# Optimization experiments

Measured on AMD Instinct MI355X. Metric: run time of the kernel, lower is better.

The kernel has to match this reference:

```python
import jax, jax.numpy as jnp
import numpy as np

B, T, E, H = 4, 1024, 1024, 16
D = E // H  # head_dim = 64


def setup_inputs() -> dict:
    key = jax.random.key(0)
    ks = jax.random.split(key, 6)
    s = 0.02  # realistic init scale for stable softmax
    return {
        "hidden_states": jax.random.normal(ks[0], (B, T, E), jnp.float32),
        "attention_mask": jnp.zeros((B, 1, T, T), jnp.float32),
        "Wq": jax.random.normal(ks[1], (E, E), jnp.float32) * s,
        "bq": jnp.zeros((E,), jnp.float32),
        "Wk": jax.random.normal(ks[2], (E, E), jnp.float32) * s,
        "bk": jnp.zeros((E,), jnp.float32),
        "Wv": jax.random.normal(ks[3], (E, E), jnp.float32) * s,
        "bv": jnp.zeros((E,), jnp.float32),
        "Wo": jax.random.normal(ks[4], (E, E), jnp.float32) * s,
        "bo": jnp.zeros((E,), jnp.float32),
    }


def reference(hidden_states, attention_mask, Wq, bq, Wk, bk, Wv, bv, Wo, bo):
    b, t, e = hidden_states.shape
    scaling = jnp.asarray(D, hidden_states.dtype) ** -0.5
    # q_proj weights/bias are pre-scaled in the module; equivalent to scaling q output
    q = (hidden_states @ Wq.T + bq) * scaling      # [B,T,E]
    k = hidden_states @ Wk.T + bk                   # self-attention path (no cache)
    v = hidden_states @ Wv.T + bv
    q = q.reshape(b, t, H, D)
    k = k.reshape(b, t, H, D)
    v = v.reshape(b, t, H, D)
    # bmm(q, k^T): [B,H,T,S] score matrix (materialized, as in the original)
    scores = jnp.einsum("bthd,bshd->bhts", q, k) + attention_mask
    probs = jax.nn.softmax(scores, axis=-1)
    ctx = jnp.einsum("bhts,bshd->bthd", probs, v).reshape(b, t, e)
    return ctx @ Wo.T + bo
```

## Files before the change

### kernel.cpp

```cpp
#include <hip/hip_runtime.h>
#include <math.h>

#define BB 4
#define TT 1024
#define EE 1024
#define HH 16
#define DD 64
#define KDIM 1024
#define N_HS (4096 * 1024)
#define N_W  (1024 * 1024)
#define NQKV (BB * HH * TT * DD)
#define LOG2E 1.44269504088896340736f

typedef _Float16 f16x8 __attribute__((ext_vector_type(8)));
typedef _Float16 f16x4 __attribute__((ext_vector_type(4)));
typedef float    f32x4 __attribute__((ext_vector_type(4)));

__device__ __forceinline__ unsigned short f2h(float x) {
    _Float16 h = (_Float16)x;
    return __builtin_bit_cast(unsigned short, h);
}
__device__ __forceinline__ void split_h(float x, unsigned short& hi, unsigned short& lo) {
    _Float16 h = (_Float16)x;
    hi = __builtin_bit_cast(unsigned short, h);
    lo = f2h(x - (float)h);
}

__device__ __forceinline__ void gload16(const void* g, void* l) {
    __builtin_amdgcn_global_load_lds(
        (const __attribute__((address_space(1))) void*)g,
        (__attribute__((address_space(3))) void*)l, 16, 0, 0);
}

__global__ __launch_bounds__(256)
void split_kernel(const float* __restrict__ hs,
                  const float* __restrict__ Wq, const float* __restrict__ Wk,
                  const float* __restrict__ Wv, const float* __restrict__ Wo,
                  unsigned short* __restrict__ ws)
{
    const int u = blockIdx.x * 256 + threadIdx.x;
    const float* src;
    unsigned short* dst;
    if (u < (N_HS / 4)) {
        src = hs + (size_t)u * 4;
        dst = ws + (size_t)u * 4;
    } else {
        int v = u - N_HS / 4;
        int wsel = v >> 18;
        int wo   = v & 0x3FFFF;
        const float* Wsrc = (wsel == 0) ? Wq : (wsel == 1) ? Wk : (wsel == 2) ? Wv : Wo;
        src = Wsrc + (size_t)wo * 4;
        dst = ws + (size_t)N_HS + (size_t)wsel * N_W + (size_t)wo * 4;
    }
    float4 x = *(const float4*)src;
    ushort4 h4;
    h4.x = f2h(x.x); h4.y = f2h(x.y); h4.z = f2h(x.z); h4.w = f2h(x.w);
    *(ushort4*)dst = h4;
}

__global__ __launch_bounds__(256)
void mtrans_kernel(const float* __restrict__ mask, float* __restrict__ mt)
{
    __shared__ float Ts[64][65];
    const int b  = blockIdx.y;
    const int m0 = (blockIdx.x & 15) * 64;
    const int n0 = (blockIdx.x >> 4) * 64;
    const float* src = mask + ((size_t)b * TT + m0) * TT + n0;
    float*       dst = mt   + ((size_t)b * TT + n0) * TT + m0;
    const int tid = threadIdx.x;
#pragma unroll
    for (int i = 0; i < 4; i++) {
        int id = tid + i * 256;
        int r = id >> 4, c = id & 15;
        float4 v = *(const float4*)(src + (size_t)r * TT + c * 4);
        Ts[r][c * 4 + 0] = v.x; Ts[r][c * 4 + 1] = v.y;
        Ts[r][c * 4 + 2] = v.z; Ts[r][c * 4 + 3] = v.w;
    }
    __syncthreads();
#pragma unroll
    for (int i = 0; i < 4; i++) {
        int id = tid + i * 256;
        int d = id >> 4, c = id & 15;
        float4 o;
        o.x = Ts[c * 4 + 0][d] * LOG2E;
        o.y = Ts[c * 4 + 1][d] * LOG2E;
        o.z = Ts[c * 4 + 2][d] * LOG2E;
        o.w = Ts[c * 4 + 3][d] * LOG2E;
        *(float4*)(dst + (size_t)d * TT + c * 4) = o;
    }
}

__global__ __launch_bounds__(256)
void qkv_kernel(const unsigned short* __restrict__ hsp,
                const unsigned short* __restrict__ wqp,
                const float* __restrict__ bq, const float* __restrict__ bk,
                const float* __restrict__ bv,
                unsigned short* __restrict__ qkvb)
{
    __shared__ unsigned short Ah[128 * 32], Bh[128 * 32];

    const int widx  = blockIdx.x >> 3;
    const int nbase = (blockIdx.x & 7) * 128;
    const int mbase = blockIdx.y * 128;
    const unsigned short* Wp = wqp + (size_t)widx * N_W;
    const float* bias = (widx == 0) ? bq : (widx == 1) ? bk : bv;
    unsigned short* dst = qkvb + (size_t)widx * NQKV;
    const float scale = (widx == 0) ? 0.125f * LOG2E : 1.0f;

    const int tid  = threadIdx.x;
    const int w    = tid >> 6;
    const int lane = tid & 63;
    const int quad = lane >> 4;
    const int l16  = lane & 15;
    const int wm   = (w >> 1) * 64;
    const int wn   = (w & 1) * 64;

    f32x4 acc[4][4];
#pragma unroll
    for (int i = 0; i < 4; i++)
#pragma unroll
        for (int j = 0; j < 4; j++) acc[i][j] = (f32x4)0.f;

#pragma unroll 1
    for (int kt = 0; kt < KDIM; kt += 32) {
        __syncthreads();
#pragma unroll
        for (int i = 0; i < 2; i++) {
            int u = tid + i * 256;
            int r = u >> 2, c = u & 3;
            int q = c ^ ((r >> 1) & 3);
            gload16(hsp + (size_t)(mbase + r) * KDIM + kt + q * 8, &Ah[u * 8]);
            gload16(Wp  + (size_t)(nbase + r) * KDIM + kt + q * 8, &Bh[u * 8]);
        }
        __syncthreads();

        f16x8 af[4], bfr[4];
#pragma unroll
        for (int i = 0; i < 4; i++) {
            int r = wm + i * 16 + l16;
            af[i] = *(const f16x8*)&Ah[(r * 4 + (quad ^ ((r >> 1) & 3))) * 8];
        }
#pragma unroll
        for (int j = 0; j < 4; j++) {
            int r = wn + j * 16 + l16;
            bfr[j] = *(const f16x8*)&Bh[(r * 4 + (quad ^ ((r >> 1) & 3))) * 8];
        }
#pragma unroll
        for (int i = 0; i < 4; i++)
#pragma unroll
            for (int j = 0; j < 4; j++)
                acc[i][j] = __builtin_amdgcn_mfma_f32_16x16x32_f16(af[i], bfr[j], acc[i][j], 0, 0, 0);
    }

#pragma unroll
    for (int j = 0; j < 4; j++) {
        int n = nbase + wn + j * 16 + l16;
        int h = n >> 6, d = n & 63;
        float bj = bias[n];
#pragma unroll
        for (int i = 0; i < 4; i++)
#pragma unroll
            for (int rr = 0; rr < 4; rr++) {
                int m = mbase + wm + i * 16 + quad * 4 + rr;
                int b = m >> 10, t = m & 1023;
                dst[(((size_t)(b * HH + h) * TT + t) * DD + d)] =
                    f2h((acc[i][j][rr] + bj) * scale);
            }
    }
}

__global__ __launch_bounds__(256)
void vtrans_kernel(const unsigned short* __restrict__ vp,
                   unsigned short* __restrict__ vtp)
{
    __shared__ unsigned short Ts[64 * 72];
    const int bh = blockIdx.y;
    const int t0 = blockIdx.x * 64;
    const unsigned short* src = vp  + (size_t)bh * TT * DD + (size_t)t0 * DD;
    unsigned short*       dst = vtp + (size_t)bh * DD * TT + t0;
    const int tid = threadIdx.x;

#pragma unroll
    for (int i = 0; i < 2; i++) {
        int id = tid + i * 256;
        int r = id >> 3, c = id & 7;
        *(uint4*)&Ts[r * 72 + c * 8] = *(const uint4*)(src + (size_t)r * DD + c * 8);
    }
    __syncthreads();
#pragma unroll
    for (int i = 0; i < 2; i++) {
        int id = tid + i * 256;
        int d = id >> 3, c = id & 7;
        unsigned short tmp[8];
#pragma unroll
        for (int j = 0; j < 8; j++) tmp[j] = Ts[(c * 8 + j) * 72 + d];
        uint4 o;
        o.x = (unsigned int)tmp[0] | ((unsigned int)tmp[1] << 16);
        o.y = (unsigned int)tmp[2] | ((unsigned int)tmp[3] << 16);
        o.z = (unsigned int)tmp[4] | ((unsigned int)tmp[5] << 16);
        o.w = (unsigned int)tmp[6] | ((unsigned int)tmp[7] << 16);
        *(uint4*)(dst + (size_t)d * TT + c * 8) = o;
    }
}

__global__ __launch_bounds__(256)
void outproj_kernel(const unsigned short* __restrict__ ctxh,
                    const unsigned short* __restrict__ ctxl,
                    const unsigned short* __restrict__ wop,
                    const float* __restrict__ bo, float* __restrict__ out)
{
    __shared__ unsigned short Ach[64 * 32], Acl[64 * 32], Bh[128 * 32];

    const int nbase = blockIdx.x * 128;
    const int mbase = blockIdx.y * 64;

    const int tid  = threadIdx.x;
    const int w    = tid >> 6;
    const int lane = tid & 63;
    const int quad = lane >> 4;
    const int l16  = lane & 15;
    const int wm   = (w >> 1) * 32;
    const int wn   = (w & 1) * 64;

    f32x4 acc[2][4];
#pragma unroll
    for (int i = 0; i < 2; i++)
#pragma unroll
        for (int j = 0; j < 4; j++) acc[i][j] = (f32x4)0.f;

#pragma unroll 1
    for (int kt = 0; kt < KDIM; kt += 32) {
        __syncthreads();
        {
            int r = tid >> 2, c = tid & 3;
            int q = c ^ ((r >> 1) & 3);
            size_t ga = (size_t)(mbase + r) * KDIM + kt + q * 8;
            gload16(ctxh + ga, &Ach[tid * 8]);
            gload16(ctxl + ga, &Acl[tid * 8]);
        }
#pragma unroll
        for (int i = 0; i < 2; i++) {
            int u = tid + i * 256;
            int r = u >> 2, c = u & 3;
            int q = c ^ ((r >> 1) & 3);
            gload16(wop + (size_t)(nbase + r) * KDIM + kt + q * 8, &Bh[u * 8]);
        }
        __syncthreads();

        f16x8 ah[2], al[2], bfr[4];
#pragma unroll
        for (int i = 0; i < 2; i++) {
            int r = wm + i * 16 + l16;
            int slot = (r * 4 + (quad ^ ((r >> 1) & 3))) * 8;
            ah[i] = *(const f16x8*)&Ach[slot];
            al[i] = *(const f16x8*)&Acl[slot];
        }
#pragma unroll
        for (int j = 0; j < 4; j++) {
            int r = wn + j * 16 + l16;
            bfr[j] = *(const f16x8*)&Bh[(r * 4 + (quad ^ ((r >> 1) & 3))) * 8];
        }
#pragma unroll
        for (int i = 0; i < 2; i++)
#pragma unroll
            for (int j = 0; j < 4; j++) {
                acc[i][j] = __builtin_amdgcn_mfma_f32_16x16x32_f16(ah[i], bfr[j], acc[i][j], 0, 0, 0);
                acc[i][j] = __builtin_amdgcn_mfma_f32_16x16x32_f16(al[i], bfr[j], acc[i][j], 0, 0, 0);
            }
    }

#pragma unroll
    for (int j = 0; j < 4; j++) {
        int n = nbase + wn + j * 16 + l16;
        float bj = bo[n];
#pragma unroll
        for (int i = 0; i < 2; i++)
#pragma unroll
            for (int rr = 0; rr < 4; rr++) {
                int m = mbase + wm + i * 16 + quad * 4 + rr;
                out[(size_t)m * EE + n] = acc[i][j][rr] + bj;
            }
    }
}

__global__ __launch_bounds__(256)
void attn_kernel(const unsigned short* __restrict__ qp_, const unsigned short* __restrict__ kp_,
                 const unsigned short* __restrict__ vtp_,
                 const float* __restrict__ mtp,
                 unsigned short* __restrict__ ctxh, unsigned short* __restrict__ ctxl)
{
    __shared__ unsigned short Ks[2][64 * 64];
    __shared__ unsigned short Vt[2][64 * 64];

    const int bh = blockIdx.y;
    const int b  = bh >> 4;
    const int h  = bh & 15;
    const int m0 = blockIdx.x * 64;
    const size_t hoff = (size_t)bh * TT * DD;
    const unsigned short* qhp = qp_ + hoff;
    const unsigned short* khp = kp_ + hoff;
    const unsigned short* vtp = vtp_ + hoff;
    const float* mb = mtp + (size_t)b * TT * TT;

    const int tid  = threadIdx.x;
    const int w    = tid >> 6;
    const int lane = tid & 63;
    const int quad = lane >> 4;
    const int l16  = lane & 15;
    const int m    = m0 + w * 16 + l16;

    f16x8 qf[2];
#pragma unroll
    for (int s = 0; s < 2; s++)
        qf[s] = *(const f16x8*)(qhp + (size_t)m * DD + s * 32 + quad * 8);

    f32x4 o2[4];
#pragma unroll
    for (int u = 0; u < 4; u++) o2[u] = (f32x4)0.f;
    float m_i = -INFINITY, l_i = 0.f;

#pragma unroll
    for (int i = 0; i < 2; i++) {
        int u = tid + i * 256;
        int r = u >> 3, cp = u & 7;
        int c = cp ^ (r & 7);
        gload16(khp + (size_t)r * DD + c * 8, &Ks[0][u * 8]);
        gload16(vtp + (size_t)r * TT + c * 8, &Vt[0][u * 8]);
    }
    __syncthreads();

#pragma unroll 2
    for (int it = 0; it < 16; ++it) {
        const int n0  = it * 64;
        const int cur = it & 1;

        f32x4 st[4];
#pragma unroll
        for (int t = 0; t < 4; t++)
#pragma unroll
            for (int r = 0; r < 4; r++)
                st[t][r] = mb[(size_t)(n0 + 16 * t + quad * 4 + r) * TT + m];

        if (it < 15) {
#pragma unroll
            for (int i = 0; i < 2; i++) {
                int u = tid + i * 256;
                int r = u >> 3, cp = u & 7;
                int c = cp ^ (r & 7);
                gload16(khp + (size_t)(n0 + 64 + r) * DD + c * 8, &Ks[cur ^ 1][u * 8]);
                gload16(vtp + (size_t)r * TT + n0 + 64 + c * 8,   &Vt[cur ^ 1][u * 8]);
            }
        }

        __builtin_amdgcn_s_setprio(1);
#pragma unroll
        for (int s = 0; s < 2; s++)
#pragma unroll
            for (int t = 0; t < 4; t++) {
                int R = 16 * t + l16;
                const f16x8 kf = *(const f16x8*)&Ks[cur][(R * 8 + ((s * 4 + quad) ^ (R & 7))) * 8];
                st[t] = __builtin_amdgcn_mfma_f32_16x16x32_f16(kf, qf[s], st[t], 0, 0, 0);
            }
        __builtin_amdgcn_s_setprio(0);

        float rm0 = fmaxf(fmaxf(st[0][0], st[0][1]), fmaxf(st[0][2], st[0][3]));
        float rm1 = fmaxf(fmaxf(st[1][0], st[1][1]), fmaxf(st[1][2], st[1][3]));
        float rm2 = fmaxf(fmaxf(st[2][0], st[2][1]), fmaxf(st[2][2], st[2][3]));
        float rm3 = fmaxf(fmaxf(st[3][0], st[3][1]), fmaxf(st[3][2], st[3][3]));
        float rm  = fmaxf(fmaxf(rm0, rm1), fmaxf(rm2, rm3));
        rm = fmaxf(rm, __shfl_xor(rm, 16));
        rm = fmaxf(rm, __shfl_xor(rm, 32));
        float mn    = fmaxf(m_i, rm);
        float alpha = exp2f(m_i - mn);
        m_i = mn;
        float rs = 0.f;
#pragma unroll
        for (int t = 0; t < 4; t++)
#pragma unroll
            for (int r = 0; r < 4; r++) {
                float p = exp2f(st[t][r] - mn);
                st[t][r] = p;
                rs += p;
            }
        rs += __shfl_xor(rs, 16);
        rs += __shfl_xor(rs, 32);
        l_i = l_i * alpha + rs;

        f16x4 pb[4];
#pragma unroll
        for (int t = 0; t < 4; t++) {
            f16x4 pv;
            pv[0] = (_Float16)st[t][0]; pv[1] = (_Float16)st[t][1];
            pv[2] = (_Float16)st[t][2]; pv[3] = (_Float16)st[t][3];
            pb[t] = pv;
        }

#pragma unroll
        for (int u = 0; u < 4; u++)
#pragma unroll
            for (int rr = 0; rr < 4; rr++) o2[u][rr] *= alpha;

        __builtin_amdgcn_s_setprio(1);
#pragma unroll
        for (int u = 0; u < 4; u++) {
            int R = 16 * u + l16;
#pragma unroll
            for (int t = 0; t < 4; t++) {
                const f16x4 vv = *(const f16x4*)&Vt[cur][(R * 8 + ((2 * t + (quad >> 1)) ^ (R & 7))) * 8 + (quad & 1) * 4];
                o2[u] = __builtin_amdgcn_mfma_f32_16x16x16f16(vv, pb[t], o2[u], 0, 0, 0);
            }
        }
        __builtin_amdgcn_s_setprio(0);

        __syncthreads();
    }

    float inv = 1.0f / l_i;
#pragma unroll
    for (int u = 0; u < 4; u++)
#pragma unroll
        for (int rr = 0; rr < 4; rr++) {
            float val = o2[u][rr] * inv;
            unsigned short hi, lo;
            split_h(val, hi, lo);
            size_t off = ((size_t)(b * TT + m)) * EE + h * DD + u * 16 + quad * 4 + rr;
            ctxh[off] = hi;
            ctxl[off] = lo;
        }
}

extern "C" void kernel_launch(void* const* d_in, const int* in_sizes, int n_in,
                              void* d_out, int out_size, void* d_ws, size_t ws_size,
                              hipStream_t stream)
{
    const float* hs   = (const float*)d_in[0];
    const float* mask = (const float*)d_in[1];
    const float* Wq   = (const float*)d_in[2];
    const float* bq   = (const float*)d_in[3];
    const float* Wk   = (const float*)d_in[4];
    const float* bk   = (const float*)d_in[5];
    const float* Wv   = (const float*)d_in[6];
    const float* bv   = (const float*)d_in[7];
    const float* Wo   = (const float*)d_in[8];
    const float* bo   = (const float*)d_in[9];
    float* out = (float*)d_out;

    unsigned short* ws   = (unsigned short*)d_ws;
    unsigned short* hsp  = ws;
    unsigned short* wqp  = ws + (size_t)N_HS;
    unsigned short* wop  = wqp + 3 * (size_t)N_W;
    unsigned short* qkvb = wqp + 4 * (size_t)N_W;
    unsigned short* qp   = qkvb;
    unsigned short* kp   = qp + (size_t)NQKV;
    unsigned short* vp   = kp + (size_t)NQKV;
    unsigned short* ctxh = ws;
    unsigned short* ctxl = qkvb + 3 * (size_t)NQKV;
    unsigned short* vtp  = ctxl + (size_t)N_HS;
    float*          mtp  = (float*)(vtp + (size_t)NQKV);

    split_kernel<<<8192, 256, 0, stream>>>(hs, Wq, Wk, Wv, Wo, ws);
    mtrans_kernel<<<dim3(256, BB), 256, 0, stream>>>(mask, mtp);
    qkv_kernel<<<dim3(24, 32), 256, 0, stream>>>(hsp, wqp, bq, bk, bv, qkvb);
    vtrans_kernel<<<dim3(TT / 64, BB * HH), 256, 0, stream>>>(vp, vtp);
    attn_kernel<<<dim3(TT / 64, BB * HH), 256, 0, stream>>>(qp, kp, vtp, mtp, ctxh, ctxl);
    outproj_kernel<<<dim3(8, 64), 256, 0, stream>>>(ctxh, ctxl, wop, bo, out);
}
```

Baseline: 233.6 us.

## Skip all-zero mask loads via runtime flag and defer softmax rescaling

Drops the separate mask-transpose kernel. The split kernel now also scans the mask and sets a device flag with atomicOr if any entry is nonzero. The attention kernel reads the flag and only loads mask values, read untransposed and scaled by log2e, when the flag is set; otherwise scores start at zero. This removes the mask transpose traffic and the per-head mask reads from the hot loop in the common zero-mask case, while the non-zero path now does strided loads. The online softmax also rescales the running max, sum and accumulator only when the new row max exceeds the old one by more than 8 in log2 units. This cuts per-tile exp and multiply work, at the cost of letting probabilities reach up to 2^8 before conversion to fp16.

After: 223.2 us. 1.05x faster.

```diff
diff --git a/kernel.cpp b/kernel.cpp
--- a/kernel.cpp
+++ b/kernel.cpp
@@ -36,57 +36,34 @@
 void split_kernel(const float* __restrict__ hs,
                   const float* __restrict__ Wq, const float* __restrict__ Wk,
                   const float* __restrict__ Wv, const float* __restrict__ Wo,
+                  const float* __restrict__ mask, int* __restrict__ mflag,
                   unsigned short* __restrict__ ws)
 {
     const int u = blockIdx.x * 256 + threadIdx.x;
-    const float* src;
-    unsigned short* dst;
-    if (u < (N_HS / 4)) {
-        src = hs + (size_t)u * 4;
-        dst = ws + (size_t)u * 4;
+    if (u < (N_HS / 4) + N_W) {
+        const float* src;
+        unsigned short* dst;
+        if (u < (N_HS / 4)) {
+            src = hs + (size_t)u * 4;
+            dst = ws + (size_t)u * 4;
+        } else {
+            int v = u - N_HS / 4;
+            int wsel = v >> 18;
+            int wo   = v & 0x3FFFF;
+            const float* Wsrc = (wsel == 0) ? Wq : (wsel == 1) ? Wk : (wsel == 2) ? Wv : Wo;
+            src = Wsrc + (size_t)wo * 4;
+            dst = ws + (size_t)N_HS + (size_t)wsel * N_W + (size_t)wo * 4;
+        }
+        float4 x = *(const float4*)src;
+        ushort4 h4;
+        h4.x = f2h(x.x); h4.y = f2h(x.y); h4.z = f2h(x.z); h4.w = f2h(x.w);
+        *(ushort4*)dst = h4;
     } else {
-        int v = u - N_HS / 4;
-        int wsel = v >> 18;
-        int wo   = v & 0x3FFFF;
-        const float* Wsrc = (wsel == 0) ? Wq : (wsel == 1) ? Wk : (wsel == 2) ? Wv : Wo;
-        src = Wsrc + (size_t)wo * 4;
-        dst = ws + (size_t)N_HS + (size_t)wsel * N_W + (size_t)wo * 4;
-    }
-    float4 x = *(const float4*)src;
-    ushort4 h4;
-    h4.x = f2h(x.x); h4.y = f2h(x.y); h4.z = f2h(x.z); h4.w = f2h(x.w);
-    *(ushort4*)dst = h4;
-}
-
-__global__ __launch_bounds__(256)
-void mtrans_kernel(const float* __restrict__ mask, float* __restrict__ mt)
-{
-    __shared__ float Ts[64][65];
-    const int b  = blockIdx.y;
-    const int m0 = (blockIdx.x & 15) * 64;
-    const int n0 = (blockIdx.x >> 4) * 64;
-    const float* src = mask + ((size_t)b * TT + m0) * TT + n0;
-    float*       dst = mt   + ((size_t)b * TT + n0) * TT + m0;
-    const int tid = threadIdx.x;
-#pragma unroll
-    for (int i = 0; i < 4; i++) {
-        int id = tid + i * 256;
-        int r = id >> 4, c = id & 15;
-        float4 v = *(const float4*)(src + (size_t)r * TT + c * 4);
-        Ts[r][c * 4 + 0] = v.x; Ts[r][c * 4 + 1] = v.y;
-        Ts[r][c * 4 + 2] = v.z; Ts[r][c * 4 + 3] = v.w;
-    }
-    __syncthreads();
-#pragma unroll
-    for (int i = 0; i < 4; i++) {
-        int id = tid + i * 256;
-        int d = id >> 4, c = id & 15;
-        float4 o;
-        o.x = Ts[c * 4 + 0][d] * LOG2E;
-        o.y = Ts[c * 4 + 1][d] * LOG2E;
-        o.z = Ts[c * 4 + 2][d] * LOG2E;
-        o.w = Ts[c * 4 + 3][d] * LOG2E;
-        *(float4*)(dst + (size_t)d * TT + c * 4) = o;
+        int v = u - ((N_HS / 4) + N_W);
+        float4 x = *(const float4*)(mask + (size_t)v * 4);
+        bool nz = (x.x != 0.f) || (x.y != 0.f) || (x.z != 0.f) || (x.w != 0.f);
+        if (__any(nz) && (threadIdx.x & 63) == 0)
+            atomicOr(mflag, 1);
     }
 }
 
@@ -286,7 +263,7 @@
 __global__ __launch_bounds__(256)
 void attn_kernel(const unsigned short* __restrict__ qp_, const unsigned short* __restrict__ kp_,
                  const unsigned short* __restrict__ vtp_,
-                 const float* __restrict__ mtp,
+                 const float* __restrict__ mask, const int* __restrict__ mflag,
                  unsigned short* __restrict__ ctxh, unsigned short* __restrict__ ctxl)
 {
     __shared__ unsigned short Ks[2][64 * 64];
@@ -300,7 +277,7 @@
     const unsigned short* qhp = qp_ + hoff;
     const unsigned short* khp = kp_ + hoff;
     const unsigned short* vtp = vtp_ + hoff;
-    const float* mb = mtp + (size_t)b * TT * TT;
+    const float* mb = mask + (size_t)b * TT * TT;
 
     const int tid  = threadIdx.x;
     const int w    = tid >> 6;
@@ -309,6 +286,8 @@
     const int l16  = lane & 15;
     const int m    = m0 + w * 16 + l16;
 
+    const int usemask = mflag[0];
+
     f16x8 qf[2];
 #pragma unroll
     for (int s = 0; s < 2; s++)
@@ -334,13 +313,6 @@
         const int n0  = it * 64;
         const int cur = it & 1;
 
-        f32x4 st[4];
-#pragma unroll
-        for (int t = 0; t < 4; t++)
-#pragma unroll
-            for (int r = 0; r < 4; r++)
-                st[t][r] = mb[(size_t)(n0 + 16 * t + quad * 4 + r) * TT + m];
-
         if (it < 15) {
 #pragma unroll
             for (int i = 0; i < 2; i++) {
@@ -352,6 +324,18 @@
             }
         }
 
+        f32x4 st[4];
+        if (usemask) {
+#pragma unroll
+            for (int t = 0; t < 4; t++)
+#pragma unroll
+                for (int r = 0; r < 4; r++)
+                    st[t][r] = mb[(size_t)m * TT + n0 + 16 * t + quad * 4 + r] * LOG2E;
+        } else {
+#pragma unroll
+            for (int t = 0; t < 4; t++) st[t] = (f32x4)0.f;
+        }
+
         __builtin_amdgcn_s_setprio(1);
 #pragma unroll
         for (int s = 0; s < 2; s++)
@@ -363,28 +347,36 @@
             }
         __builtin_amdgcn_s_setprio(0);
 
-        float rm0 = fmaxf(fmaxf(st[0][0], st[0][1]), fmaxf(st[0][2], st[0][3]));
-        float rm1 = fmaxf(fmaxf(st[1][0], st[1][1]), fmaxf(st[1][2], st[1][3]));
-        float rm2 = fmaxf(fmaxf(st[2][0], st[2][1]), fmaxf(st[2][2], st[2][3]));
-        float rm3 = fmaxf(fmaxf(st[3][0], st[3][1]), fmaxf(st[3][2], st[3][3]));
-        float rm  = fmaxf(fmaxf(rm0, rm1), fmaxf(rm2, rm3));
+        float rm = fmaxf(fmaxf(fmaxf(st[0][0], st[0][1]), fmaxf(st[0][2], st[0][3])),
+                         fmaxf(fmaxf(st[1][0], st[1][1]), fmaxf(st[1][2], st[1][3])));
+        rm = fmaxf(rm, fmaxf(fmaxf(st[2][0], st[2][1]), fmaxf(st[2][2], st[2][3])));
+        rm = fmaxf(rm, fmaxf(fmaxf(st[3][0], st[3][1]), fmaxf(st[3][2], st[3][3])));
         rm = fmaxf(rm, __shfl_xor(rm, 16));
         rm = fmaxf(rm, __shfl_xor(rm, 32));
-        float mn    = fmaxf(m_i, rm);
-        float alpha = exp2f(m_i - mn);
-        m_i = mn;
+
+        if (__any(rm > m_i + 8.f)) {
+            float mn    = fmaxf(m_i, rm);
+            float alpha = exp2f(m_i - mn);
+            m_i = mn;
+            l_i *= alpha;
+#pragma unroll
+            for (int u = 0; u < 4; u++)
+#pragma unroll
+                for (int rr = 0; rr < 4; rr++) o2[u][rr] *= alpha;
+        }
+
         float rs = 0.f;
 #pragma unroll
         for (int t = 0; t < 4; t++)
 #pragma unroll
             for (int r = 0; r < 4; r++) {
-                float p = exp2f(st[t][r] - mn);
+                float p = exp2f(st[t][r] - m_i);
                 st[t][r] = p;
                 rs += p;
             }
         rs += __shfl_xor(rs, 16);
         rs += __shfl_xor(rs, 32);
-        l_i = l_i * alpha + rs;
+        l_i += rs;
 
         f16x4 pb[4];
 #pragma unroll
@@ -394,11 +386,6 @@
             pv[2] = (_Float16)st[t][2]; pv[3] = (_Float16)st[t][3];
             pb[t] = pv;
         }
-
-#pragma unroll
-        for (int u = 0; u < 4; u++)
-#pragma unroll
-            for (int rr = 0; rr < 4; rr++) o2[u][rr] *= alpha;
 
         __builtin_amdgcn_s_setprio(1);
 #pragma unroll
@@ -456,12 +443,12 @@
     unsigned short* ctxh = ws;
     unsigned short* ctxl = qkvb + 3 * (size_t)NQKV;
     unsigned short* vtp  = ctxl + (size_t)N_HS;
-    float*          mtp  = (float*)(vtp + (size_t)NQKV);
-
-    split_kernel<<<8192, 256, 0, stream>>>(hs, Wq, Wk, Wv, Wo, ws);
-    mtrans_kernel<<<dim3(256, BB), 256, 0, stream>>>(mask, mtp);
+    int*            mflag = (int*)(vtp + (size_t)NQKV);
+
+    hipMemsetAsync(mflag, 0, sizeof(int), stream);
+    split_kernel<<<12288, 256, 0, stream>>>(hs, Wq, Wk, Wv, Wo, mask, mflag, ws);
     qkv_kernel<<<dim3(24, 32), 256, 0, stream>>>(hsp, wqp, bq, bk, bv, qkvb);
     vtrans_kernel<<<dim3(TT / 64, BB * HH), 256, 0, stream>>>(vp, vtp);
-    attn_kernel<<<dim3(TT / 64, BB * HH), 256, 0, stream>>>(qp, kp, vtp, mtp, ctxh, ctxl);
+    attn_kernel<<<dim3(TT / 64, BB * HH), 256, 0, stream>>>(qp, kp, vtp, mask, mflag, ctxh, ctxl);
     outproj_kernel<<<dim3(8, 64), 256, 0, stream>>>(ctxh, ctxl, wop, bo, out);
 }
```
